# Kernel tuning notes

Hardware: AMD Instinct MI355X
Metric: run time of the kernel (lower is better)

## Reference

```python
import jax, jax.numpy as jnp
import numpy as np

B, S, D = 2, 2048, 1024
H, DA, DL = 8, 64, 64   # heads, attention_dim, linear_dim
L = 2                    # num_blocks


def _layernorm(x, w, b, eps):
    mu = jnp.mean(x, axis=-1, keepdims=True)
    var = jnp.mean(jnp.square(x - mu), axis=-1, keepdims=True)
    return (x - mu) * jax.lax.rsqrt(var + eps) * w + b


def _norm_no_affine(x, eps):
    mu = jnp.mean(x, axis=-1, keepdims=True)
    var = jnp.mean(jnp.square(x - mu), axis=-1, keepdims=True)
    return (x - mu) * jax.lax.rsqrt(var + eps)


def setup_inputs() -> dict:
    key = jax.random.key(0)
    ks = jax.random.split(key, 8)
    x = jax.random.normal(ks[0], (B, S, D), dtype=jnp.float32)
    # causal visibility mask: True = visible
    attn_mask = jnp.tril(jnp.ones((S, S), dtype=bool))[None].repeat(B, axis=0)
    proj_dim = DL * 2 * H + DA * 2 * H  # 2048
    uvqk = jax.random.normal(ks[1], (L, D, proj_dim), dtype=jnp.float32) * 0.02
    o_w = jax.random.normal(ks[2], (L, D, DL * H), dtype=jnp.float32) * 0.02  # torch [out,in]
    o_b = jnp.zeros((L, D), dtype=jnp.float32)
    ln_w = jnp.ones((L, D), dtype=jnp.float32)
    ln_b = jnp.zeros((L, D), dtype=jnp.float32)
    last_ln_w = jnp.ones((D,), dtype=jnp.float32)
    last_ln_b = jnp.zeros((D,), dtype=jnp.float32)
    return {"x": x, "attn_mask": attn_mask, "uvqk": uvqk, "o_w": o_w,
            "o_b": o_b, "ln_w": ln_w, "ln_b": ln_b,
            "last_ln_w": last_ln_w, "last_ln_b": last_ln_b}


def reference(x, attn_mask, uvqk, o_w, o_b, ln_w, ln_b, last_ln_w, last_ln_b):
    seq_len = x.shape[1]
    m = attn_mask[:, None, :, :]  # [B,1,S,S]
    for i in range(L):
        h = _layernorm(x, ln_w[i], ln_b[i], 1e-6)                 # [B,S,D]
        proj = jax.nn.silu(jnp.einsum('bsd,de->bse', h, uvqk[i]))  # [B,S,2*(DL+DA)*H]
        u, v, q, k = jnp.split(proj, [DL * H, 2 * DL * H, 2 * DL * H + DA * H], axis=-1)
        q = q.reshape(B, seq_len, H, DA).transpose(0, 2, 1, 3)   # [B,H,S,DA]
        kk = k.reshape(B, seq_len, H, DA).transpose(0, 2, 1, 3)
        vv = v.reshape(B, seq_len, H, DL).transpose(0, 2, 1, 3)  # [B,H,S,DL]
        uu = u.reshape(B, seq_len, H, DL).transpose(0, 2, 1, 3)
        scores = jnp.einsum('bhsd,bhtd->bhst', q, kk)            # [B,H,S,S]
        scores = jnp.where(m, jax.nn.silu(scores) / seq_len, 0.0)
        out = jnp.einsum('bhst,bhtd->bhsd', scores, vv)          # [B,H,S,DL]
        out = _norm_no_affine(out, 1e-6)
        u_dot = (uu * out).transpose(0, 2, 1, 3).reshape(B, seq_len, DL * H)
        x = x + jnp.einsum('bsf,df->bsd', u_dot, o_w[i]) + o_b[i]
    return _layernorm(x, last_ln_w, last_ln_b, 1e-8)
```

## Files before the change

kernel.cpp:

```cpp
#include <hip/hip_runtime.h>

#define B_ 2
#define S_ 2048
#define D_ 1024
#define H_ 8
#define L_ 2
#define P_ 2048
#define F_ 512
#define R_ (B_*S_)

typedef unsigned short u16;
typedef unsigned int u32;
typedef __bf16 bf16;
typedef bf16 bf16x8 __attribute__((ext_vector_type(8)));
typedef short short8 __attribute__((ext_vector_type(8)));
typedef float v4f __attribute__((ext_vector_type(4)));

__device__ __forceinline__ float silu_fast(float x){
  float e = __expf(-x);
  return x * __builtin_amdgcn_rcpf(1.0f + e);
}
__device__ __forceinline__ float bf2f(u16 u){
  union { u32 i; float f; } x; x.i = ((u32)u) << 16; return x.f;
}
__device__ __forceinline__ u16 f2bfu(float f){
  union { float f; u32 i; } x; x.f = f;
  u32 r = x.i + 0x7fff + ((x.i >> 16) & 1);
  return (u16)(r >> 16);
}

__global__ __launch_bounds__(256) void cvt_owh_kernel(const float* __restrict__ src, u16* __restrict__ dst){
  int i = (blockIdx.x * 256 + threadIdx.x) * 4;
  float4 v = *(const float4*)(src + i);
  int l = i >> 19;
  int rem = i & ((1 << 19) - 1);
  int n = rem >> 9, f = rem & 511;
  int ng = n >> 4, l15 = n & 15;
  int c = f >> 5, q = (f >> 3) & 3, j = f & 7;
  ushort4 o; o.x = f2bfu(v.x); o.y = f2bfu(v.y); o.z = f2bfu(v.z); o.w = f2bfu(v.w);
  *(ushort4*)(dst + (size_t)l * D_ * F_ + ((size_t)(c*64 + ng))*512 + q*128 + l15*8 + j) = o;
}

__global__ __launch_bounds__(256) void cvt_uvqkT_kernel(const float* __restrict__ uvqk, u16* __restrict__ ot){
  __shared__ float t[32][33];
  int l = blockIdx.z;
  int p0 = blockIdx.x * 32, d0 = blockIdx.y * 32;
  int tx = threadIdx.x & 31, ty = threadIdx.x >> 5;
  const float* src = uvqk + ((size_t)l * D_ + d0) * P_ + p0;
  #pragma unroll
  for (int s = 0; s < 4; s++)
    t[ty + s*8][tx] = src[(size_t)(ty + s*8) * P_ + tx];
  __syncthreads();
  u16* dstl = ot + (size_t)l * P_ * D_;
  #pragma unroll
  for (int s = 0; s < 4; s++){
    int p = p0 + ty + s*8;
    int d = d0 + tx;
    int ng = p >> 4, l15 = p & 15;
    int c = d >> 5, q = (d >> 3) & 3, j = d & 7;
    dstl[((size_t)(c*128 + ng))*512 + q*128 + l15*8 + j] = f2bfu(t[tx][ty + s*8]);
  }
}

__global__ __launch_bounds__(256) void kvpack_kernel(const u16* __restrict__ projh,
    u16* __restrict__ kpack, u16* __restrict__ vpack){
  __shared__ u16 tls[64*72];
  int t = blockIdx.x, t0 = t * 64;
  int bh = blockIdx.y;
  int b = bh >> 3, hh = bh & 7;
  int tid = threadIdx.x;
  const size_t bS = (size_t)b * S_;
  const int voff = F_ + hh*64, koff = 3*F_ + hh*64;
  {
    int row = tid >> 2, c16 = (tid & 3) * 16;
    const u16* sp = projh + (bS + t0 + row) * P_ + voff + c16;
    short8 a = *(const short8*)sp;
    short8 bq = *(const short8*)(sp + 8);
    *(short8*)&tls[row*72 + c16] = a;
    *(short8*)&tls[row*72 + c16 + 8] = bq;
  }
  __syncthreads();
  size_t obase = ((size_t)(bh*32 + t) * 8) * 512;
  #pragma unroll
  for (int pass = 0; pass < 2; pass++){
    int id = tid + pass * 256;
    int c = id >> 6, lane = id & 63;
    int quad = lane >> 4, l15 = lane & 15;
    int cns = c >> 1, ckst = c & 1;
    const u16* kp = projh + (bS + t0 + cns*16 + l15) * P_ + koff + ckst*32 + quad*8;
    *(short8*)(kpack + obase + (size_t)c*512 + lane*8) = *(const short8*)kp;
    short8 vv;
    #pragma unroll
    for (int j = 0; j < 8; j++)
      vv[j] = (short)tls[(ckst*32 + quad*8 + j)*72 + cns*16 + l15];
    *(short8*)(vpack + obase + (size_t)c*512 + lane*8) = vv;
  }
}

__global__ __launch_bounds__(256) void ln_kernel(const float* __restrict__ src,
    const float* __restrict__ w, const float* __restrict__ b,
    void* __restrict__ outp, float eps, int out_bf16){
  int row = blockIdx.x, tid = threadIdx.x;
  const float* xr = src + (size_t)row * D_;
  float4 v = *(const float4*)(xr + tid * 4);
  float s  = v.x + v.y + v.z + v.w;
  float sq = v.x*v.x + v.y*v.y + v.z*v.z + v.w*v.w;
  #pragma unroll
  for (int off = 32; off; off >>= 1){ s += __shfl_down(s, off); sq += __shfl_down(sq, off); }
  __shared__ float red[8];
  __shared__ float stats[2];
  int wid = tid >> 6;
  if ((tid & 63) == 0){ red[wid] = s; red[4 + wid] = sq; }
  __syncthreads();
  if (tid == 0){
    float S1 = red[0] + red[1] + red[2] + red[3];
    float S2 = red[4] + red[5] + red[6] + red[7];
    float mu = S1 * (1.0f / D_);
    float var = S2 * (1.0f / D_) - mu * mu;
    stats[0] = mu; stats[1] = rsqrtf(var + eps);
  }
  __syncthreads();
  float mu = stats[0], rs = stats[1];
  int i = tid * 4;
  float4 wv = *(const float4*)(w + i);
  float4 bv = *(const float4*)(b + i);
  float o0 = (v.x - mu) * rs * wv.x + bv.x;
  float o1 = (v.y - mu) * rs * wv.y + bv.y;
  float o2 = (v.z - mu) * rs * wv.z + bv.z;
  float o3 = (v.w - mu) * rs * wv.w + bv.w;
  if (out_bf16){
    ushort4 o; o.x = f2bfu(o0); o.y = f2bfu(o1); o.z = f2bfu(o2); o.w = f2bfu(o3);
    int mg = row >> 4, l15 = row & 15;
    int c = i >> 5, q = (i >> 3) & 3, j = i & 7;
    *(ushort4*)((u16*)outp + ((size_t)(c*256 + mg))*512 + q*128 + l15*8 + j) = o;
  } else {
    *(float4*)((float*)outp + (size_t)row * D_ + i) = make_float4(o0, o1, o2, o3);
  }
}

template<int KCH, int MGA, int MGB>
__device__ __forceinline__ void gemm_pk_core(const u16* __restrict__ Ap,
    const u16* __restrict__ Bp, int mg0, int ng0, v4f acc[4][4]){
  int lane = threadIdx.x & 63;
  const u16* ap = Ap + (size_t)mg0*512 + lane*8;
  const u16* bp = Bp + (size_t)ng0*512 + lane*8;
  short8 aA[4], bA[4], aB[4], bB[4];
  auto LOADK = [&](short8 (&af)[4], short8 (&bf)[4], int c){
    const u16* apc = ap + (size_t)c*MGA*512;
    const u16* bpc = bp + (size_t)c*MGB*512;
    #pragma unroll
    for (int i = 0; i < 4; i++){
      af[i] = *(const short8*)(apc + i*512);
      bf[i] = *(const short8*)(bpc + i*512);
    }
  };
  auto COMP = [&](const short8 (&af)[4], const short8 (&bf)[4]){
    #pragma unroll
    for (int i = 0; i < 4; i++)
      #pragma unroll
      for (int j = 0; j < 4; j++)
        acc[i][j] = __builtin_amdgcn_mfma_f32_16x16x32_bf16(
            __builtin_bit_cast(bf16x8, af[i]), __builtin_bit_cast(bf16x8, bf[j]),
            acc[i][j], 0, 0, 0);
  };
  LOADK(aA, bA, 0);
  for (int c = 0; c < KCH; c += 2){
    LOADK(aB, bB, c + 1);
    COMP(aA, bA);
    if (c + 2 < KCH) LOADK(aA, bA, c + 2);
    COMP(aB, bB);
  }
}

__global__ __launch_bounds__(256) void gemm_silu_mfma(const u16* __restrict__ A,
    const u16* __restrict__ Bt, u16* __restrict__ C){
  v4f acc[4][4];
  #pragma unroll
  for (int i = 0; i < 4; i++)
    #pragma unroll
    for (int j = 0; j < 4; j++) acc[i][j] = (v4f){0.f,0.f,0.f,0.f};
  int f = blockIdx.x;
  int k = f & 7, local = f >> 3;
  int by = (k & 3) * 8 + (local >> 3);
  int bx = (k >> 2) * 8 + (local & 7);
  int m0 = by * 128, n0 = bx * 128;
  int tid = threadIdx.x, w = tid >> 6, lane = tid & 63;
  int wm = w >> 1, wn = w & 1, quad = lane >> 4, l15 = lane & 15;
  gemm_pk_core<32, 256, 128>(A, Bt, (m0 >> 4) + wm*4, (n0 >> 4) + wn*4, acc);
  #pragma unroll
  for (int i = 0; i < 4; i++)
    #pragma unroll
    for (int r = 0; r < 4; r++){
      int m = m0 + wm*64 + i*16 + quad*4 + r;
      u16* cp = C + (size_t)m * P_ + n0 + wn*64 + l15;
      #pragma unroll
      for (int j = 0; j < 4; j++)
        cp[j*16] = f2bfu(silu_fast(acc[i][j][r]));
    }
}

__global__ __launch_bounds__(256) void gemm_add_mfma(const u16* __restrict__ A,
    const u16* __restrict__ Bt, const float* __restrict__ bias,
    const float* __restrict__ Xin, float* __restrict__ Xout){
  v4f acc[4][4];
  #pragma unroll
  for (int i = 0; i < 4; i++)
    #pragma unroll
    for (int j = 0; j < 4; j++) acc[i][j] = (v4f){0.f,0.f,0.f,0.f};
  int f = blockIdx.x;
  int k = f & 7, local = f >> 3;
  int by = (k & 3) * 8 + (local >> 2);
  int bx = (k >> 2) * 4 + (local & 3);
  int m0 = by * 128, n0 = bx * 128;
  int tid = threadIdx.x, w = tid >> 6, lane = tid & 63;
  int wm = w >> 1, wn = w & 1, quad = lane >> 4, l15 = lane & 15;
  gemm_pk_core<16, 256, 64>(A, Bt, (m0 >> 4) + wm*4, (n0 >> 4) + wn*4, acc);
  float bj[4];
  #pragma unroll
  for (int j = 0; j < 4; j++) bj[j] = bias[n0 + wn*64 + j*16 + l15];
  #pragma unroll
  for (int i = 0; i < 4; i++)
    #pragma unroll
    for (int r = 0; r < 4; r++){
      int m = m0 + wm*64 + i*16 + quad*4 + r;
      size_t off = (size_t)m * D_ + n0 + wn*64 + l15;
      const float* xi = Xin + off;
      float* xo = Xout + off;
      #pragma unroll
      for (int j = 0; j < 4; j++)
        xo[j*16] = xi[j*16] + acc[i][j][r] + bj[j];
    }
}

__global__ __launch_bounds__(256) void attn_kernel(const u16* __restrict__ projh,
                                                   const u16* __restrict__ kpack,
                                                   const u16* __restrict__ vpack,
                                                   u16* __restrict__ opart){
  __shared__ u16 Ps[64*72];
  int f = (int)blockIdx.x;
  int g = f & 7;
  int s = f >> 3;
  int c = s & 31;
  int slot = s >> 5;
  int z = c >> 4;
  int x = c & 15;
  int qt = slot ? x : (15 - x);
  int bh = g + (slot << 3);
  int ttop = 2*qt + 1;
  int b = bh >> 3, hh = bh & 7;
  int tid = threadIdx.x;
  int w = tid >> 6, lane = tid & 63, quad = lane >> 4, l15 = lane & 15;
  int s0 = qt * 128;
  const size_t bS = (size_t)b * S_;
  const int qoff = 2*F_ + hh*64;

  bf16x8 aq[2][2];
  #pragma unroll
  for (int qh = 0; qh < 2; qh++){
    const u16* qp = projh + (bS + s0 + qh*64 + w*16 + l15) * P_ + qoff + quad*8;
    aq[qh][0] = __builtin_bit_cast(bf16x8, *(const short8*)qp);
    aq[qh][1] = __builtin_bit_cast(bf16x8, *(const short8*)(qp + 32));
  }

  v4f oacc[2][4];
  #pragma unroll
  for (int qh = 0; qh < 2; qh++)
    #pragma unroll
    for (int i = 0; i < 4; i++) oacc[qh][i] = (v4f){0.f, 0.f, 0.f, 0.f};

  auto LOADT = [&](short8 (&BK)[4][2], short8 (&VF)[4][2], int tt){
    size_t pb = ((size_t)(bh*32 + tt) * 8) * 512;
    #pragma unroll
    for (int cc = 0; cc < 8; cc++){
      BK[cc>>1][cc&1] = *(const short8*)(kpack + pb + (size_t)cc*512 + lane*8);
      VF[cc>>1][cc&1] = *(const short8*)(vpack + pb + (size_t)cc*512 + lane*8);
    }
  };

  auto COMPUTE = [&](const short8 (&BK)[4][2], const short8 (&VF)[4][2], int t){
    #pragma unroll
    for (int qh = 0; qh < 2; qh++){
      int dtile = 2*qt + qh;
      if (t > dtile) continue;
      v4f sacc[4];
      #pragma unroll
      for (int i = 0; i < 4; i++) sacc[i] = (v4f){0.f, 0.f, 0.f, 0.f};
      #pragma unroll
      for (int ns = 0; ns < 4; ns++){
        sacc[ns] = __builtin_amdgcn_mfma_f32_16x16x32_bf16(aq[qh][0],
            __builtin_bit_cast(bf16x8, BK[ns][0]), sacc[ns], 0, 0, 0);
        sacc[ns] = __builtin_amdgcn_mfma_f32_16x16x32_bf16(aq[qh][1],
            __builtin_bit_cast(bf16x8, BK[ns][1]), sacc[ns], 0, 0, 0);
      }
      bool diag = (t == dtile);
      #pragma unroll
      for (int ns = 0; ns < 4; ns++){
        #pragma unroll
        for (int r = 0; r < 4; r++){
          int rl = w*16 + quad*4 + r;
          int cl = ns*16 + l15;
          float p = silu_fast(sacc[ns][r]) * (1.0f / S_);
          if (diag && cl > rl) p = 0.0f;
          Ps[rl*72 + cl] = f2bfu(p);
        }
      }
      #pragma unroll
      for (int kst = 0; kst < 2; kst++){
        short8 aps = *(const short8*)&Ps[(w*16 + l15)*72 + kst*32 + quad*8];
        bf16x8 ap = __builtin_bit_cast(bf16x8, aps);
        #pragma unroll
        for (int ds = 0; ds < 4; ds++)
          oacc[qh][ds] = __builtin_amdgcn_mfma_f32_16x16x32_bf16(
              ap, __builtin_bit_cast(bf16x8, VF[ds][kst]), oacc[qh][ds], 0, 0, 0);
      }
    }
  };

  short8 kA[4][2], vA[4][2], kB[4][2], vB[4][2];
  int t = z;
  LOADT(kA, vA, t);
  for (;;){
    if (t + 2 <= ttop){
      LOADT(kB, vB, t + 2);
      COMPUTE(kA, vA, t);
      t += 2;
    } else {
      COMPUTE(kA, vA, t);
      break;
    }
    if (t + 2 <= ttop){
      LOADT(kA, vA, t + 2);
      COMPUTE(kB, vB, t);
      t += 2;
    } else {
      COMPUTE(kB, vB, t);
      break;
    }
  }

  u16* ob = opart + (size_t)z * ((size_t)R_ * F_);
  #pragma unroll
  for (int qh = 0; qh < 2; qh++){
    #pragma unroll
    for (int r = 0; r < 4; r++){
      int sg = s0 + qh*64 + w*16 + quad*4 + r;
      u16* op = ob + (bS + sg) * (size_t)F_ + hh*64 + l15;
      #pragma unroll
      for (int ds = 0; ds < 4; ds++)
        op[ds*16] = f2bfu(oacc[qh][ds][r]);
    }
  }
}

__global__ __launch_bounds__(256) void norm_gate_kernel(const u16* __restrict__ opart,
    const u16* __restrict__ projh, u16* __restrict__ udot){
  int w = threadIdx.x >> 6, lane = threadIdx.x & 63;
  int sg = blockIdx.x * 4 + w;
  int hh = lane >> 3, seg = lane & 7;
  size_t off = (size_t)sg * F_ + hh*64 + seg*8;
  short8 a0 = *(const short8*)(opart + off);
  short8 a1 = *(const short8*)(opart + (size_t)R_ * F_ + off);
  float e[8];
  float s = 0.f, sq = 0.f;
  #pragma unroll
  for (int i = 0; i < 8; i++){
    e[i] = bf2f((u16)a0[i]) + bf2f((u16)a1[i]);
    s += e[i]; sq += e[i]*e[i];
  }
  #pragma unroll
  for (int m = 1; m < 8; m <<= 1){
    s  += __shfl_xor(s, m, 64);
    sq += __shfl_xor(sq, m, 64);
  }
  float mu = s * (1.0f/64.0f);
  float var = sq * (1.0f/64.0f) - mu*mu;
  float rs = rsqrtf(var + 1e-6f);
  const u16* up = projh + (size_t)sg * P_ + hh*64 + seg*8;
  short8 uv = *(const short8*)up;
  short8 ov;
  #pragma unroll
  for (int i = 0; i < 8; i++)
    ov[i] = (short)f2bfu((e[i] - mu) * rs * bf2f((u16)uv[i]));
  int mg = sg >> 4, l15 = sg & 15;
  int c = hh*2 + (seg >> 2), q = seg & 3;
  *(short8*)(udot + ((size_t)(c*256 + mg))*512 + q*128 + l15*8) = ov;
}

extern "C" void kernel_launch(void* const* d_in, const int* in_sizes, int n_in,
                              void* d_out, int out_size, void* d_ws, size_t ws_size,
                              hipStream_t stream){
  (void)in_sizes; (void)n_in; (void)out_size; (void)ws_size;
  const float* x     = (const float*)d_in[0];
  const float* uvqk  = (const float*)d_in[2];
  const float* o_w   = (const float*)d_in[3];
  const float* o_b   = (const float*)d_in[4];
  const float* ln_w  = (const float*)d_in[5];
  const float* ln_b  = (const float*)d_in[6];
  const float* lln_w = (const float*)d_in[7];
  const float* lln_b = (const float*)d_in[8];
  float* out = (float*)d_out;

  char* ws = (char*)d_ws;
  float* xf    = (float*)ws;
  u16*   h     = (u16*)(ws + (16u<<20));
  u16*   kpack = h;
  u16*   vpack = (u16*)(ws + (20u<<20));
  u16*   udot  = (u16*)(ws + (24u<<20));
  u16*   projh = (u16*)(ws + (28u<<20));
  u16*   uvqkT = (u16*)(ws + (44u<<20));
  u16*   owh   = (u16*)(ws + (52u<<20));
  u16*   opart = (u16*)(ws + (54u<<20));

  cvt_uvqkT_kernel<<<dim3(P_/32, D_/32, L_), 256, 0, stream>>>(uvqk, uvqkT);
  cvt_owh_kernel<<<L_ * D_ * F_ / 1024, 256, 0, stream>>>(o_w, owh);
  for (int l = 0; l < L_; l++){
    const float* xsrc = (l == 0) ? x : xf;
    ln_kernel<<<R_, 256, 0, stream>>>(xsrc, ln_w + l * D_, ln_b + l * D_, h, 1e-6f, 1);
    gemm_silu_mfma<<<512, 256, 0, stream>>>(
        h, uvqkT + (size_t)l * P_ * D_, projh);
    kvpack_kernel<<<dim3(S_/64, B_*H_), 256, 0, stream>>>(projh, kpack, vpack);
    attn_kernel<<<512, 256, 0, stream>>>(projh, kpack, vpack, opart);
    norm_gate_kernel<<<R_/4, 256, 0, stream>>>(opart, projh, udot);
    gemm_add_mfma<<<256, 256, 0, stream>>>(
        udot, owh + (size_t)l * D_ * F_, o_b + l * D_, xsrc, xf);
  }
  ln_kernel<<<R_, 256, 0, stream>>>(xf, lln_w, lln_b, out, 1e-8f, 0);
}
```

Before: 296.3 us.

## Shrink GEMM output tiles to launch more blocks and vectorize weight transpose stores

Templates the packed MFMA GEMM core on per-wave tile counts. The QKV/UV projection GEMM moves to 128x64 tiles with 1024 blocks, and the output GEMM moves to 64x64 tiles with 1024 blocks, so more blocks cover the MI355X compute units. The weight-transpose conversion kernel now writes contiguous ushort4 chunks of the packed layout instead of scattered scalar stores. Smaller tiles lower per-block operand reuse and raise global/L2 traffic in exchange for better occupancy and load balance.

```diff
diff --git a/kernel.cpp b/kernel.cpp
--- a/kernel.cpp
+++ b/kernel.cpp
@@ -51,15 +51,17 @@
   for (int s = 0; s < 4; s++)
     t[ty + s*8][tx] = src[(size_t)(ty + s*8) * P_ + tx];
   __syncthreads();
-  u16* dstl = ot + (size_t)l * P_ * D_;
-  #pragma unroll
-  for (int s = 0; s < 4; s++){
-    int p = p0 + ty + s*8;
-    int d = d0 + tx;
-    int ng = p >> 4, l15 = p & 15;
-    int c = d >> 5, q = (d >> 3) & 3, j = d & 7;
-    dstl[((size_t)(c*128 + ng))*512 + q*128 + l15*8 + j] = f2bfu(t[tx][ty + s*8]);
-  }
+  int o = threadIdx.x * 4;
+  int ngl = o >> 9, rem = o & 511;
+  int q = rem >> 7, l15 = (rem >> 3) & 15, j0 = rem & 7;
+  int pl = ngl*16 + l15;
+  ushort4 ov;
+  ov.x = f2bfu(t[q*8 + j0 + 0][pl]);
+  ov.y = f2bfu(t[q*8 + j0 + 1][pl]);
+  ov.z = f2bfu(t[q*8 + j0 + 2][pl]);
+  ov.w = f2bfu(t[q*8 + j0 + 3][pl]);
+  size_t base = ((size_t)(blockIdx.y*128 + blockIdx.x*2))*512;
+  *(ushort4*)(ot + (size_t)l * P_ * D_ + base + o) = ov;
 }
 
 __global__ __launch_bounds__(256) void kvpack_kernel(const u16* __restrict__ projh,
@@ -138,27 +140,26 @@
   }
 }
 
-template<int KCH, int MGA, int MGB>
+template<int KCH, int MGA, int MGB, int NI, int NJ>
 __device__ __forceinline__ void gemm_pk_core(const u16* __restrict__ Ap,
-    const u16* __restrict__ Bp, int mg0, int ng0, v4f acc[4][4]){
+    const u16* __restrict__ Bp, int mg0, int ng0, v4f (&acc)[NI][NJ]){
   int lane = threadIdx.x & 63;
   const u16* ap = Ap + (size_t)mg0*512 + lane*8;
   const u16* bp = Bp + (size_t)ng0*512 + lane*8;
-  short8 aA[4], bA[4], aB[4], bB[4];
-  auto LOADK = [&](short8 (&af)[4], short8 (&bf)[4], int c){
+  short8 aA[NI], bA[NJ], aB[NI], bB[NJ];
+  auto LOADK = [&](short8 (&af)[NI], short8 (&bf)[NJ], int c){
     const u16* apc = ap + (size_t)c*MGA*512;
     const u16* bpc = bp + (size_t)c*MGB*512;
     #pragma unroll
-    for (int i = 0; i < 4; i++){
-      af[i] = *(const short8*)(apc + i*512);
-      bf[i] = *(const short8*)(bpc + i*512);
-    }
+    for (int i = 0; i < NI; i++) af[i] = *(const short8*)(apc + i*512);
+    #pragma unroll
+    for (int j = 0; j < NJ; j++) bf[j] = *(const short8*)(bpc + j*512);
   };
-  auto COMP = [&](const short8 (&af)[4], const short8 (&bf)[4]){
-    #pragma unroll
-    for (int i = 0; i < 4; i++)
-      #pragma unroll
-      for (int j = 0; j < 4; j++)
+  auto COMP = [&](const short8 (&af)[NI], const short8 (&bf)[NJ]){
+    #pragma unroll
+    for (int i = 0; i < NI; i++)
+      #pragma unroll
+      for (int j = 0; j < NJ; j++)
         acc[i][j] = __builtin_amdgcn_mfma_f32_16x16x32_bf16(
             __builtin_bit_cast(bf16x8, af[i]), __builtin_bit_cast(bf16x8, bf[j]),
             acc[i][j], 0, 0, 0);
@@ -174,27 +175,27 @@
 
 __global__ __launch_bounds__(256) void gemm_silu_mfma(const u16* __restrict__ A,
     const u16* __restrict__ Bt, u16* __restrict__ C){
-  v4f acc[4][4];
+  v4f acc[4][2];
   #pragma unroll
   for (int i = 0; i < 4; i++)
     #pragma unroll
-    for (int j = 0; j < 4; j++) acc[i][j] = (v4f){0.f,0.f,0.f,0.f};
+    for (int j = 0; j < 2; j++) acc[i][j] = (v4f){0.f,0.f,0.f,0.f};
   int f = blockIdx.x;
   int k = f & 7, local = f >> 3;
-  int by = (k & 3) * 8 + (local >> 3);
-  int bx = (k >> 2) * 8 + (local & 7);
-  int m0 = by * 128, n0 = bx * 128;
+  int by = (k & 3) * 8 + (local >> 4);
+  int bx = (k >> 2) * 16 + (local & 15);
+  int m0 = by * 128, n0 = bx * 64;
   int tid = threadIdx.x, w = tid >> 6, lane = tid & 63;
   int wm = w >> 1, wn = w & 1, quad = lane >> 4, l15 = lane & 15;
-  gemm_pk_core<32, 256, 128>(A, Bt, (m0 >> 4) + wm*4, (n0 >> 4) + wn*4, acc);
+  gemm_pk_core<32, 256, 128, 4, 2>(A, Bt, (m0 >> 4) + wm*4, (n0 >> 4) + wn*2, acc);
   #pragma unroll
   for (int i = 0; i < 4; i++)
     #pragma unroll
     for (int r = 0; r < 4; r++){
       int m = m0 + wm*64 + i*16 + quad*4 + r;
-      u16* cp = C + (size_t)m * P_ + n0 + wn*64 + l15;
-      #pragma unroll
-      for (int j = 0; j < 4; j++)
+      u16* cp = C + (size_t)m * P_ + n0 + wn*32 + l15;
+      #pragma unroll
+      for (int j = 0; j < 2; j++)
         cp[j*16] = f2bfu(silu_fast(acc[i][j][r]));
     }
 }
@@ -202,32 +203,32 @@
 __global__ __launch_bounds__(256) void gemm_add_mfma(const u16* __restrict__ A,
     const u16* __restrict__ Bt, const float* __restrict__ bias,
     const float* __restrict__ Xin, float* __restrict__ Xout){
-  v4f acc[4][4];
-  #pragma unroll
-  for (int i = 0; i < 4; i++)
-    #pragma unroll
-    for (int j = 0; j < 4; j++) acc[i][j] = (v4f){0.f,0.f,0.f,0.f};
+  v4f acc[2][2];
+  #pragma unroll
+  for (int i = 0; i < 2; i++)
+    #pragma unroll
+    for (int j = 0; j < 2; j++) acc[i][j] = (v4f){0.f,0.f,0.f,0.f};
   int f = blockIdx.x;
   int k = f & 7, local = f >> 3;
-  int by = (k & 3) * 8 + (local >> 2);
-  int bx = (k >> 2) * 4 + (local & 3);
-  int m0 = by * 128, n0 = bx * 128;
+  int by = (k & 3) * 16 + (local >> 3);
+  int bx = (k >> 2) * 8 + (local & 7);
+  int m0 = by * 64, n0 = bx * 64;
   int tid = threadIdx.x, w = tid >> 6, lane = tid & 63;
   int wm = w >> 1, wn = w & 1, quad = lane >> 4, l15 = lane & 15;
-  gemm_pk_core<16, 256, 64>(A, Bt, (m0 >> 4) + wm*4, (n0 >> 4) + wn*4, acc);
-  float bj[4];
-  #pragma unroll
-  for (int j = 0; j < 4; j++) bj[j] = bias[n0 + wn*64 + j*16 + l15];
-  #pragma unroll
-  for (int i = 0; i < 4; i++)
+  gemm_pk_core<16, 256, 64, 2, 2>(A, Bt, (m0 >> 4) + wm*2, (n0 >> 4) + wn*2, acc);
+  float bj[2];
+  #pragma unroll
+  for (int j = 0; j < 2; j++) bj[j] = bias[n0 + wn*32 + j*16 + l15];
+  #pragma unroll
+  for (int i = 0; i < 2; i++)
     #pragma unroll
     for (int r = 0; r < 4; r++){
-      int m = m0 + wm*64 + i*16 + quad*4 + r;
-      size_t off = (size_t)m * D_ + n0 + wn*64 + l15;
+      int m = m0 + wm*32 + i*16 + quad*4 + r;
+      size_t off = (size_t)m * D_ + n0 + wn*32 + l15;
       const float* xi = Xin + off;
       float* xo = Xout + off;
       #pragma unroll
-      for (int j = 0; j < 4; j++)
+      for (int j = 0; j < 2; j++)
         xo[j*16] = xi[j*16] + acc[i][j][r] + bj[j];
     }
 }
@@ -416,12 +417,12 @@
   for (int l = 0; l < L_; l++){
     const float* xsrc = (l == 0) ? x : xf;
     ln_kernel<<<R_, 256, 0, stream>>>(xsrc, ln_w + l * D_, ln_b + l * D_, h, 1e-6f, 1);
-    gemm_silu_mfma<<<512, 256, 0, stream>>>(
+    gemm_silu_mfma<<<1024, 256, 0, stream>>>(
         h, uvqkT + (size_t)l * P_ * D_, projh);
     kvpack_kernel<<<dim3(S_/64, B_*H_), 256, 0, stream>>>(projh, kpack, vpack);
     attn_kernel<<<512, 256, 0, stream>>>(projh, kpack, vpack, opart);
     norm_gate_kernel<<<R_/4, 256, 0, stream>>>(opart, projh, udot);
-    gemm_add_mfma<<<256, 256, 0, stream>>>(
+    gemm_add_mfma<<<1024, 256, 0, stream>>>(
         udot, owh + (size_t)l * D_ * F_, o_b + l * D_, xsrc, xf);
   }
   ln_kernel<<<R_, 256, 0, stream>>>(xf, lln_w, lln_b, out, 1e-8f, 0);
```

Result: no change. 301.5 us (+1.8%).
